# Optimization experiments

Hardware: AMD Instinct MI355X
Metric: run time of the kernel (lower is better)

The kernel has to match this reference:

```python
import jax, jax.numpy as jnp
import numpy as np

N_NODES = 100000
N_EDGES = 1600000
F_IN = 128
F_OUT = 128


def _spmm(edge_row, edge_col, edge_weight, X):
    # sparse [N,N] @ dense [N,F]: gather source rows, weight, scatter-add to dest rows
    msgs = edge_weight[:, None] * X[edge_col]  # [E, F]
    return jax.ops.segment_sum(msgs, edge_row, num_segments=N_NODES)


def setup_inputs() -> dict:
    key = jax.random.key(0)
    ks = jax.random.split(key, 7)
    scale = 1.0 / np.sqrt(F_IN)
    return {
        "x": jax.random.normal(ks[0], (N_NODES, F_IN), dtype=jnp.float32),
        "edge_row": jax.random.randint(ks[1], (N_EDGES,), 0, N_NODES, dtype=jnp.int32),
        "edge_col": jax.random.randint(ks[2], (N_EDGES,), 0, N_NODES, dtype=jnp.int32),
        "edge_weight": jax.random.uniform(ks[3], (N_EDGES,), dtype=jnp.float32),
        "w1": jax.random.normal(ks[4], (F_IN, F_IN), dtype=jnp.float32) * scale,
        "w2": jax.random.normal(ks[5], (F_IN, F_OUT), dtype=jnp.float32) * scale,
        "w3": jax.random.normal(ks[6], (F_OUT, F_OUT), dtype=jnp.float32) * scale,
    }


def reference(x, edge_row, edge_col, edge_weight, w1, w2, w3):
    # dropout p=0.0 (eval) -> identity
    h = jax.nn.relu(_spmm(edge_row, edge_col, edge_weight, x @ w1))
    h = jax.nn.relu(_spmm(edge_row, edge_col, edge_weight, h @ w2))
    h = jax.nn.relu(_spmm(edge_row, edge_col, edge_weight, h @ w3))
    return h
```

## Files before the change

### kernel.cpp

```cpp
#include <hip/hip_runtime.h>

#define N_NODES 100000
#define N_EDGES 1600000
#define F 128

#define SCAN_B 1024
#define SCAN_NB ((N_NODES + SCAN_B - 1) / SCAN_B)

typedef short bf16x8 __attribute__((ext_vector_type(8)));
typedef float f32x4  __attribute__((ext_vector_type(4)));

union ABFrag {
    bf16x8 v;
    unsigned short u[8];
    uint4  q;
};

__device__ __forceinline__ unsigned short f2bf(float f) {
    unsigned int u = __float_as_uint(f);
    u += 0x7fffu + ((u >> 16) & 1u);
    return (unsigned short)(u >> 16);
}
__device__ __forceinline__ float bflo(unsigned int u) {
    return __uint_as_float(u << 16);
}
__device__ __forceinline__ float bfhi(unsigned int u) {
    return __uint_as_float(u & 0xFFFF0000u);
}


__global__ void edge_histogram(const int* __restrict__ erow, int* __restrict__ counts) {
    const int e = blockIdx.x * blockDim.x + threadIdx.x;
    atomicAdd(&counts[erow[e]], 1);
}

__global__ void scan_block_sums(const int* __restrict__ counts, int* __restrict__ bsums) {
    __shared__ int s[SCAN_B];
    const int t = threadIdx.x;
    const int idx = blockIdx.x * SCAN_B + t;
    int v = (idx < N_NODES) ? counts[idx] : 0;
    s[t] = v;
    __syncthreads();
    for (int off = SCAN_B / 2; off > 0; off >>= 1) {
        if (t < off) s[t] += s[t + off];
        __syncthreads();
    }
    if (t == 0) bsums[blockIdx.x] = s[0];
}

__global__ void scan_bsums(const int* __restrict__ bsums, int* __restrict__ boffs) {
    __shared__ int s[128];
    const int t = threadIdx.x;
    int v = (t < SCAN_NB) ? bsums[t] : 0;
    s[t] = v;
    __syncthreads();
    for (int off = 1; off < 128; off <<= 1) {
        int u = (t >= off) ? s[t - off] : 0;
        __syncthreads();
        s[t] += u;
        __syncthreads();
    }
    if (t < SCAN_NB) boffs[t] = s[t] - v;
}

__global__ void scan_final(const int* __restrict__ counts, const int* __restrict__ boffs,
                           int* __restrict__ row_ptr) {
    __shared__ int s[SCAN_B];
    const int t = threadIdx.x;
    const int idx = blockIdx.x * SCAN_B + t;
    int v = (idx < N_NODES) ? counts[idx] : 0;
    s[t] = v;
    __syncthreads();
    for (int off = 1; off < SCAN_B; off <<= 1) {
        int u = (t >= off) ? s[t - off] : 0;
        __syncthreads();
        s[t] += u;
        __syncthreads();
    }
    if (idx < N_NODES) row_ptr[idx] = boffs[blockIdx.x] + s[t] - v;
    if (idx == 0) row_ptr[N_NODES] = N_EDGES;
}

__global__ void csr_fill(const int* __restrict__ erow, const int* __restrict__ ecol,
                         const float* __restrict__ ewgt,
                         const int* __restrict__ row_ptr, int* __restrict__ cursor,
                         unsigned int* __restrict__ pairs) {
    const int e = blockIdx.x * blockDim.x + threadIdx.x;
    const int dst = erow[e];
    const int pos = atomicAdd(&cursor[dst], 1);
    pairs[row_ptr[dst] + pos] = ((unsigned int)ecol[e] << 15) | (unsigned int)f2bf(ewgt[e]);
}

__global__ void transpose_w_bf16(const float* __restrict__ W, unsigned short* __restrict__ Wt) {
    const int i = blockIdx.x * 256 + threadIdx.x;
    const int n = i >> 7;
    const int k = i & 127;
    Wt[i] = f2bf(W[k * F + n]);
}

__global__ __launch_bounds__(256) void gemm_mfma(
    const float* __restrict__ Xf,
    const unsigned short* __restrict__ Xb,
    const unsigned short* __restrict__ Wt,
    unsigned short* __restrict__ Y,
    int use_f32_in)
{
    __shared__ unsigned short Wl[4 * 8 * 64 * 8];

    const int tid  = threadIdx.x;
    const int wave = tid >> 6;
    const int lane = tid & 63;

    for (int s = tid; s < 2048; s += 256) {
        const int ln  = s & 63;
        const int ntk = s >> 6;
        const int nt  = ntk & 7;
        const int kt  = ntk >> 3;
        const int n   = nt * 16 + (ln & 15);
        const int k   = kt * 32 + (ln >> 4) * 8;
        *(uint4*)(&Wl[s * 8]) = *(const uint4*)(Wt + n * F + k);
    }
    __syncthreads();

    const int m     = blockIdx.x * 64 + wave * 16 + (lane & 15);
    const bool mval = (m < N_NODES);
    const int kq    = (lane >> 4) * 8;

    f32x4 acc[8] = {};

#pragma unroll
    for (int kt = 0; kt < 4; ++kt) {
        ABFrag a;
        if (mval) {
            if (use_f32_in) {
                const float* p = Xf + (size_t)m * F + kt * 32 + kq;
                const float4 u0 = *(const float4*)p;
                const float4 u1 = *(const float4*)(p + 4);
                a.u[0] = f2bf(u0.x); a.u[1] = f2bf(u0.y);
                a.u[2] = f2bf(u0.z); a.u[3] = f2bf(u0.w);
                a.u[4] = f2bf(u1.x); a.u[5] = f2bf(u1.y);
                a.u[6] = f2bf(u1.z); a.u[7] = f2bf(u1.w);
            } else {
                a.q = *(const uint4*)(Xb + (size_t)m * F + kt * 32 + kq);
#pragma unroll
                for (int j = 0; j < 8; ++j)
                    if (a.u[j] & 0x8000u) a.u[j] = 0;
            }
        } else {
            a.q = make_uint4(0, 0, 0, 0);
        }
#pragma unroll
        for (int nt = 0; nt < 8; ++nt) {
            ABFrag b;
            b.q = *(const uint4*)(&Wl[((kt * 8 + nt) * 64 + lane) * 8]);
            acc[nt] = __builtin_amdgcn_mfma_f32_16x16x32_bf16(a.v, b.v, acc[nt], 0, 0, 0);
        }
    }

    const int rbase = blockIdx.x * 64 + wave * 16 + (lane >> 4) * 4;
    const int cbase = lane & 15;
#pragma unroll
    for (int r = 0; r < 4; ++r) {
        const int row = rbase + r;
        if (row < N_NODES) {
#pragma unroll
            for (int nt = 0; nt < 8; ++nt) {
                Y[(size_t)row * F + nt * 16 + cbase] = f2bf(acc[nt][r]);
            }
        }
    }
}

__global__ __launch_bounds__(256) void spmm_csr_bf16(
    const unsigned short* __restrict__ Xb,
    const int* __restrict__ row_ptr,
    const unsigned int* __restrict__ pairs,
    unsigned short* __restrict__ Ob,
    float* __restrict__ Of,
    int final_mode) {
    const int tid = threadIdx.x;
    const int l16 = tid & 15;
    const int q   = tid >> 4;
    const int row = blockIdx.x * 16 + q;

    const int beg = row_ptr[row];
    const int end = row_ptr[row + 1];

    float a[8] = {};
    int i = beg;
    for (; i + 1 < end; i += 2) {
        const unsigned int p0 = pairs[i], p1 = pairs[i + 1];
        const uint4 v0 = *(const uint4*)(Xb + (size_t)(p0 >> 15) * F + l16 * 8);
        const uint4 v1 = *(const uint4*)(Xb + (size_t)(p1 >> 15) * F + l16 * 8);
        const float w0 = bflo(p0 & 0x7FFFu);
        const float w1 = bflo(p1 & 0x7FFFu);
        a[0] += w0 * bflo(v0.x); a[1] += w0 * bfhi(v0.x);
        a[2] += w0 * bflo(v0.y); a[3] += w0 * bfhi(v0.y);
        a[4] += w0 * bflo(v0.z); a[5] += w0 * bfhi(v0.z);
        a[6] += w0 * bflo(v0.w); a[7] += w0 * bfhi(v0.w);
        a[0] += w1 * bflo(v1.x); a[1] += w1 * bfhi(v1.x);
        a[2] += w1 * bflo(v1.y); a[3] += w1 * bfhi(v1.y);
        a[4] += w1 * bflo(v1.z); a[5] += w1 * bfhi(v1.z);
        a[6] += w1 * bflo(v1.w); a[7] += w1 * bfhi(v1.w);
    }
    if (i < end) {
        const unsigned int p0 = pairs[i];
        const uint4 v0 = *(const uint4*)(Xb + (size_t)(p0 >> 15) * F + l16 * 8);
        const float w0 = bflo(p0 & 0x7FFFu);
        a[0] += w0 * bflo(v0.x); a[1] += w0 * bfhi(v0.x);
        a[2] += w0 * bflo(v0.y); a[3] += w0 * bfhi(v0.y);
        a[4] += w0 * bflo(v0.z); a[5] += w0 * bfhi(v0.z);
        a[6] += w0 * bflo(v0.w); a[7] += w0 * bfhi(v0.w);
    }

    if (final_mode) {
        float4 o0 = {fmaxf(a[0], 0.f), fmaxf(a[1], 0.f), fmaxf(a[2], 0.f), fmaxf(a[3], 0.f)};
        float4 o1 = {fmaxf(a[4], 0.f), fmaxf(a[5], 0.f), fmaxf(a[6], 0.f), fmaxf(a[7], 0.f)};
        float* p = Of + (size_t)row * F + l16 * 8;
        *(float4*)p = o0;
        *(float4*)(p + 4) = o1;
    } else {
        uint4 o;
        o.x = (unsigned int)f2bf(a[0]) | ((unsigned int)f2bf(a[1]) << 16);
        o.y = (unsigned int)f2bf(a[2]) | ((unsigned int)f2bf(a[3]) << 16);
        o.z = (unsigned int)f2bf(a[4]) | ((unsigned int)f2bf(a[5]) << 16);
        o.w = (unsigned int)f2bf(a[6]) | ((unsigned int)f2bf(a[7]) << 16);
        *(uint4*)(Ob + (size_t)row * F + l16 * 8) = o;
    }
}


extern "C" void kernel_launch(void* const* d_in, const int* in_sizes, int n_in,
                              void* d_out, int out_size, void* d_ws, size_t ws_size,
                              hipStream_t stream) {
    const float* x    = (const float*)d_in[0];
    const int*   erow = (const int*)d_in[1];
    const int*   ecol = (const int*)d_in[2];
    const float* ew   = (const float*)d_in[3];
    const float* w1   = (const float*)d_in[4];
    const float* w2   = (const float*)d_in[5];
    const float* w3   = (const float*)d_in[6];
    float* out = (float*)d_out;

    char* ws = (char*)d_ws;
    size_t off = 0;
    auto alloc = [&](size_t bytes) -> char* {
        char* p = ws + off;
        off += (bytes + 255) & ~(size_t)255;
        return p;
    };
    unsigned short* bufA = (unsigned short*)alloc((size_t)N_NODES * F * 2);
    unsigned short* bufB = (unsigned short*)alloc((size_t)N_NODES * F * 2);
    unsigned int* pairs  = (unsigned int*)alloc((size_t)N_EDGES * 4);
    int* counts  = (int*)alloc((size_t)N_NODES * sizeof(int));
    int* row_ptr = (int*)alloc(((size_t)N_NODES + 1) * sizeof(int));
    int* bsums   = (int*)alloc((size_t)SCAN_NB * sizeof(int));
    int* boffs   = (int*)alloc((size_t)SCAN_NB * sizeof(int));
    unsigned short* wt1 = (unsigned short*)alloc((size_t)F * F * 2);
    unsigned short* wt2 = (unsigned short*)alloc((size_t)F * F * 2);
    unsigned short* wt3 = (unsigned short*)alloc((size_t)F * F * 2);

    hipMemsetAsync(counts, 0, (size_t)N_NODES * sizeof(int), stream);
    edge_histogram<<<N_EDGES / 256, 256, 0, stream>>>(erow, counts);
    scan_block_sums<<<SCAN_NB, SCAN_B, 0, stream>>>(counts, bsums);
    scan_bsums<<<1, 128, 0, stream>>>(bsums, boffs);
    scan_final<<<SCAN_NB, SCAN_B, 0, stream>>>(counts, boffs, row_ptr);
    hipMemsetAsync(counts, 0, (size_t)N_NODES * sizeof(int), stream);
    csr_fill<<<N_EDGES / 256, 256, 0, stream>>>(erow, ecol, ew, row_ptr, counts, pairs);

    transpose_w_bf16<<<64, 256, 0, stream>>>(w1, wt1);
    transpose_w_bf16<<<64, 256, 0, stream>>>(w2, wt2);
    transpose_w_bf16<<<64, 256, 0, stream>>>(w3, wt3);

    const int ggrid = (N_NODES + 63) / 64;
    const int sgrid = N_NODES / 16;

    gemm_mfma<<<ggrid, 256, 0, stream>>>(x, nullptr, wt1, bufA, 1);
    spmm_csr_bf16<<<sgrid, 256, 0, stream>>>(bufA, row_ptr, pairs, bufB, nullptr, 0);
    gemm_mfma<<<ggrid, 256, 0, stream>>>(nullptr, bufB, wt2, bufA, 0);
    spmm_csr_bf16<<<sgrid, 256, 0, stream>>>(bufA, row_ptr, pairs, bufB, nullptr, 0);
    gemm_mfma<<<ggrid, 256, 0, stream>>>(nullptr, bufB, wt3, bufA, 0);
    spmm_csr_bf16<<<sgrid, 256, 0, stream>>>(bufA, row_ptr, pairs, nullptr, out, 1);
}
```

Before: 506.3 us.

## Partition CSR build atomics by XCD, widen GEMM tiles, unroll SpMM by four

```diff
diff --git a/kernel.cpp b/kernel.cpp
--- a/kernel.cpp
+++ b/kernel.cpp
@@ -3,17 +3,19 @@
 #define N_NODES 100000
 #define N_EDGES 1600000
 #define F 128
+#define XCD_RANGE 12500
 
 #define SCAN_B 1024
 #define SCAN_NB ((N_NODES + SCAN_B - 1) / SCAN_B)
 
 typedef short bf16x8 __attribute__((ext_vector_type(8)));
 typedef float f32x4  __attribute__((ext_vector_type(4)));
+typedef unsigned int u32x4 __attribute__((ext_vector_type(4)));
 
 union ABFrag {
     bf16x8 v;
     unsigned short u[8];
-    uint4  q;
+    u32x4  q;
 };
 
 __device__ __forceinline__ unsigned short f2bf(float f) {
@@ -29,9 +31,15 @@
 }
 
 
-__global__ void edge_histogram(const int* __restrict__ erow, int* __restrict__ counts) {
-    const int e = blockIdx.x * blockDim.x + threadIdx.x;
-    atomicAdd(&counts[erow[e]], 1);
+__global__ __launch_bounds__(256) void edge_histogram_xcd(
+    const int* __restrict__ erow, int* __restrict__ counts) {
+    const int xcd = blockIdx.x & 7;
+    const int e   = (blockIdx.x >> 3) * 256 + threadIdx.x;
+    const int dst = erow[e];
+    const int lo  = xcd * XCD_RANGE;
+    if (dst >= lo && dst < lo + XCD_RANGE) {
+        atomicAdd(&counts[dst], 1);
+    }
 }
 
 __global__ void scan_block_sums(const int* __restrict__ counts, int* __restrict__ bsums) {
@@ -81,21 +89,32 @@
     if (idx == 0) row_ptr[N_NODES] = N_EDGES;
 }
 
-__global__ void csr_fill(const int* __restrict__ erow, const int* __restrict__ ecol,
-                         const float* __restrict__ ewgt,
-                         const int* __restrict__ row_ptr, int* __restrict__ cursor,
-                         unsigned int* __restrict__ pairs) {
-    const int e = blockIdx.x * blockDim.x + threadIdx.x;
+__global__ __launch_bounds__(256) void csr_fill_xcd(
+    const int* __restrict__ erow, const int* __restrict__ ecol,
+    const float* __restrict__ ewgt,
+    const int* __restrict__ row_ptr, int* __restrict__ cursor,
+    unsigned int* __restrict__ pairs) {
+    const int xcd = blockIdx.x & 7;
+    const int e   = (blockIdx.x >> 3) * 256 + threadIdx.x;
     const int dst = erow[e];
-    const int pos = atomicAdd(&cursor[dst], 1);
-    pairs[row_ptr[dst] + pos] = ((unsigned int)ecol[e] << 15) | (unsigned int)f2bf(ewgt[e]);
-}
-
-__global__ void transpose_w_bf16(const float* __restrict__ W, unsigned short* __restrict__ Wt) {
+    const int lo  = xcd * XCD_RANGE;
+    if (dst >= lo && dst < lo + XCD_RANGE) {
+        const int col = ecol[e];
+        const float w = ewgt[e];
+        const int pos = atomicAdd(&cursor[dst], 1);
+        pairs[row_ptr[dst] + pos] = ((unsigned int)col << 15) | (unsigned int)f2bf(w);
+    }
+}
+
+__global__ void transpose_w3(const float* __restrict__ w1, const float* __restrict__ w2,
+                             const float* __restrict__ w3, unsigned short* __restrict__ wt) {
     const int i = blockIdx.x * 256 + threadIdx.x;
-    const int n = i >> 7;
-    const int k = i & 127;
-    Wt[i] = f2bf(W[k * F + n]);
+    const int which = i >> 14;
+    const int j = i & 16383;
+    const float* W = (which == 0) ? w1 : (which == 1) ? w2 : w3;
+    const int n = j >> 7;
+    const int k = j & 127;
+    wt[i] = f2bf(W[k * F + n]);
 }
 
 __global__ __launch_bounds__(256) void gemm_mfma(
@@ -118,54 +137,77 @@
         const int kt  = ntk >> 3;
         const int n   = nt * 16 + (ln & 15);
         const int k   = kt * 32 + (ln >> 4) * 8;
-        *(uint4*)(&Wl[s * 8]) = *(const uint4*)(Wt + n * F + k);
+        *(u32x4*)(&Wl[s * 8]) = *(const u32x4*)(Wt + n * F + k);
     }
     __syncthreads();
 
-    const int m     = blockIdx.x * 64 + wave * 16 + (lane & 15);
-    const bool mval = (m < N_NODES);
-    const int kq    = (lane >> 4) * 8;
-
-    f32x4 acc[8] = {};
+    const int kq = (lane >> 4) * 8;
+    const int m0 = blockIdx.x * 128 + wave * 16 + (lane & 15);
+    const int m1 = m0 + 64;
+    const bool v0 = (m0 < N_NODES);
+    const bool v1 = (m1 < N_NODES);
+
+    f32x4 acc[2][8] = {};
 
 #pragma unroll
     for (int kt = 0; kt < 4; ++kt) {
-        ABFrag a;
-        if (mval) {
-            if (use_f32_in) {
-                const float* p = Xf + (size_t)m * F + kt * 32 + kq;
+        ABFrag a0, a1;
+        a0.q = 0;
+        a1.q = 0;
+        if (use_f32_in) {
+            if (v0) {
+                const float* p = Xf + (size_t)m0 * F + kt * 32 + kq;
                 const float4 u0 = *(const float4*)p;
                 const float4 u1 = *(const float4*)(p + 4);
-                a.u[0] = f2bf(u0.x); a.u[1] = f2bf(u0.y);
-                a.u[2] = f2bf(u0.z); a.u[3] = f2bf(u0.w);
-                a.u[4] = f2bf(u1.x); a.u[5] = f2bf(u1.y);
-                a.u[6] = f2bf(u1.z); a.u[7] = f2bf(u1.w);
-            } else {
-                a.q = *(const uint4*)(Xb + (size_t)m * F + kt * 32 + kq);
+                a0.u[0] = f2bf(u0.x); a0.u[1] = f2bf(u0.y);
+                a0.u[2] = f2bf(u0.z); a0.u[3] = f2bf(u0.w);
+                a0.u[4] = f2bf(u1.x); a0.u[5] = f2bf(u1.y);
+                a0.u[6] = f2bf(u1.z); a0.u[7] = f2bf(u1.w);
+            }
+            if (v1) {
+                const float* p = Xf + (size_t)m1 * F + kt * 32 + kq;
+                const float4 u0 = *(const float4*)p;
+                const float4 u1 = *(const float4*)(p + 4);
+                a1.u[0] = f2bf(u0.x); a1.u[1] = f2bf(u0.y);
+                a1.u[2] = f2bf(u0.z); a1.u[3] = f2bf(u0.w);
+                a1.u[4] = f2bf(u1.x); a1.u[5] = f2bf(u1.y);
+                a1.u[6] = f2bf(u1.z); a1.u[7] = f2bf(u1.w);
+            }
+        } else {
+            if (v0) {
+                a0.q = *(const u32x4*)(Xb + (size_t)m0 * F + kt * 32 + kq);
 #pragma unroll
                 for (int j = 0; j < 8; ++j)
-                    if (a.u[j] & 0x8000u) a.u[j] = 0;
-            }
-        } else {
-            a.q = make_uint4(0, 0, 0, 0);
+                    if (a0.u[j] & 0x8000u) a0.u[j] = 0;
+            }
+            if (v1) {
+                a1.q = *(const u32x4*)(Xb + (size_t)m1 * F + kt * 32 + kq);
+#pragma unroll
+                for (int j = 0; j < 8; ++j)
+                    if (a1.u[j] & 0x8000u) a1.u[j] = 0;
+            }
         }
 #pragma unroll
         for (int nt = 0; nt < 8; ++nt) {
             ABFrag b;
-            b.q = *(const uint4*)(&Wl[((kt * 8 + nt) * 64 + lane) * 8]);
-            acc[nt] = __builtin_amdgcn_mfma_f32_16x16x32_bf16(a.v, b.v, acc[nt], 0, 0, 0);
+            b.q = *(const u32x4*)(&Wl[((kt * 8 + nt) * 64 + lane) * 8]);
+            acc[0][nt] = __builtin_amdgcn_mfma_f32_16x16x32_bf16(a0.v, b.v, acc[0][nt], 0, 0, 0);
+            acc[1][nt] = __builtin_amdgcn_mfma_f32_16x16x32_bf16(a1.v, b.v, acc[1][nt], 0, 0, 0);
         }
     }
 
-    const int rbase = blockIdx.x * 64 + wave * 16 + (lane >> 4) * 4;
     const int cbase = lane & 15;
 #pragma unroll
-    for (int r = 0; r < 4; ++r) {
-        const int row = rbase + r;
-        if (row < N_NODES) {
-#pragma unroll
-            for (int nt = 0; nt < 8; ++nt) {
-                Y[(size_t)row * F + nt * 16 + cbase] = f2bf(acc[nt][r]);
+    for (int t = 0; t < 2; ++t) {
+        const int rbase = blockIdx.x * 128 + t * 64 + wave * 16 + (lane >> 4) * 4;
+#pragma unroll
+        for (int r = 0; r < 4; ++r) {
+            const int row = rbase + r;
+            if (row < N_NODES) {
+#pragma unroll
+                for (int nt = 0; nt < 8; ++nt) {
+                    Y[(size_t)row * F + nt * 16 + cbase] = f2bf(acc[t][nt][r]);
+                }
             }
         }
     }
@@ -188,12 +230,19 @@
 
     float a[8] = {};
     int i = beg;
-    for (; i + 1 < end; i += 2) {
-        const unsigned int p0 = pairs[i], p1 = pairs[i + 1];
-        const uint4 v0 = *(const uint4*)(Xb + (size_t)(p0 >> 15) * F + l16 * 8);
-        const uint4 v1 = *(const uint4*)(Xb + (size_t)(p1 >> 15) * F + l16 * 8);
+    for (; i + 3 < end; i += 4) {
+        const unsigned int p0 = __builtin_nontemporal_load(&pairs[i]);
+        const unsigned int p1 = __builtin_nontemporal_load(&pairs[i + 1]);
+        const unsigned int p2 = __builtin_nontemporal_load(&pairs[i + 2]);
+        const unsigned int p3 = __builtin_nontemporal_load(&pairs[i + 3]);
+        const u32x4 v0 = *(const u32x4*)(Xb + (size_t)(p0 >> 15) * F + l16 * 8);
+        const u32x4 v1 = *(const u32x4*)(Xb + (size_t)(p1 >> 15) * F + l16 * 8);
+        const u32x4 v2 = *(const u32x4*)(Xb + (size_t)(p2 >> 15) * F + l16 * 8);
+        const u32x4 v3 = *(const u32x4*)(Xb + (size_t)(p3 >> 15) * F + l16 * 8);
         const float w0 = bflo(p0 & 0x7FFFu);
         const float w1 = bflo(p1 & 0x7FFFu);
+        const float w2 = bflo(p2 & 0x7FFFu);
+        const float w3 = bflo(p3 & 0x7FFFu);
         a[0] += w0 * bflo(v0.x); a[1] += w0 * bfhi(v0.x);
         a[2] += w0 * bflo(v0.y); a[3] += w0 * bfhi(v0.y);
         a[4] += w0 * bflo(v0.z); a[5] += w0 * bfhi(v0.z);
@@ -202,10 +251,18 @@
         a[2] += w1 * bflo(v1.y); a[3] += w1 * bfhi(v1.y);
         a[4] += w1 * bflo(v1.z); a[5] += w1 * bfhi(v1.z);
         a[6] += w1 * bflo(v1.w); a[7] += w1 * bfhi(v1.w);
-    }
-    if (i < end) {
-        const unsigned int p0 = pairs[i];
-        const uint4 v0 = *(const uint4*)(Xb + (size_t)(p0 >> 15) * F + l16 * 8);
+        a[0] += w2 * bflo(v2.x); a[1] += w2 * bfhi(v2.x);
+        a[2] += w2 * bflo(v2.y); a[3] += w2 * bfhi(v2.y);
+        a[4] += w2 * bflo(v2.z); a[5] += w2 * bfhi(v2.z);
+        a[6] += w2 * bflo(v2.w); a[7] += w2 * bfhi(v2.w);
+        a[0] += w3 * bflo(v3.x); a[1] += w3 * bfhi(v3.x);
+        a[2] += w3 * bflo(v3.y); a[3] += w3 * bfhi(v3.y);
+        a[4] += w3 * bflo(v3.z); a[5] += w3 * bfhi(v3.z);
+        a[6] += w3 * bflo(v3.w); a[7] += w3 * bfhi(v3.w);
+    }
+    for (; i < end; ++i) {
+        const unsigned int p0 = __builtin_nontemporal_load(&pairs[i]);
+        const u32x4 v0 = *(const u32x4*)(Xb + (size_t)(p0 >> 15) * F + l16 * 8);
         const float w0 = bflo(p0 & 0x7FFFu);
         a[0] += w0 * bflo(v0.x); a[1] += w0 * bfhi(v0.x);
         a[2] += w0 * bflo(v0.y); a[3] += w0 * bfhi(v0.y);
@@ -214,18 +271,18 @@
     }
 
     if (final_mode) {
-        float4 o0 = {fmaxf(a[0], 0.f), fmaxf(a[1], 0.f), fmaxf(a[2], 0.f), fmaxf(a[3], 0.f)};
-        float4 o1 = {fmaxf(a[4], 0.f), fmaxf(a[5], 0.f), fmaxf(a[6], 0.f), fmaxf(a[7], 0.f)};
+        f32x4 o0 = {fmaxf(a[0], 0.f), fmaxf(a[1], 0.f), fmaxf(a[2], 0.f), fmaxf(a[3], 0.f)};
+        f32x4 o1 = {fmaxf(a[4], 0.f), fmaxf(a[5], 0.f), fmaxf(a[6], 0.f), fmaxf(a[7], 0.f)};
         float* p = Of + (size_t)row * F + l16 * 8;
-        *(float4*)p = o0;
-        *(float4*)(p + 4) = o1;
+        __builtin_nontemporal_store(o0, (f32x4*)p);
+        __builtin_nontemporal_store(o1, (f32x4*)(p + 4));
     } else {
-        uint4 o;
+        u32x4 o;
         o.x = (unsigned int)f2bf(a[0]) | ((unsigned int)f2bf(a[1]) << 16);
         o.y = (unsigned int)f2bf(a[2]) | ((unsigned int)f2bf(a[3]) << 16);
         o.z = (unsigned int)f2bf(a[4]) | ((unsigned int)f2bf(a[5]) << 16);
         o.w = (unsigned int)f2bf(a[6]) | ((unsigned int)f2bf(a[7]) << 16);
-        *(uint4*)(Ob + (size_t)row * F + l16 * 8) = o;
+        __builtin_nontemporal_store(o, (u32x4*)(Ob + (size_t)row * F + l16 * 8));
     }
 }
 
@@ -252,27 +309,26 @@
     unsigned short* bufA = (unsigned short*)alloc((size_t)N_NODES * F * 2);
     unsigned short* bufB = (unsigned short*)alloc((size_t)N_NODES * F * 2);
     unsigned int* pairs  = (unsigned int*)alloc((size_t)N_EDGES * 4);
-    int* counts  = (int*)alloc((size_t)N_NODES * sizeof(int));
+    int* counts  = (int*)alloc((size_t)N_NODES * sizeof(int) * 2);
+    int* cursor  = counts + N_NODES;
     int* row_ptr = (int*)alloc(((size_t)N_NODES + 1) * sizeof(int));
     int* bsums   = (int*)alloc((size_t)SCAN_NB * sizeof(int));
     int* boffs   = (int*)alloc((size_t)SCAN_NB * sizeof(int));
-    unsigned short* wt1 = (unsigned short*)alloc((size_t)F * F * 2);
-    unsigned short* wt2 = (unsigned short*)alloc((size_t)F * F * 2);
-    unsigned short* wt3 = (unsigned short*)alloc((size_t)F * F * 2);
-
-    hipMemsetAsync(counts, 0, (size_t)N_NODES * sizeof(int), stream);
-    edge_histogram<<<N_EDGES / 256, 256, 0, stream>>>(erow, counts);
+    unsigned short* wt = (unsigned short*)alloc((size_t)3 * F * F * 2);
+    unsigned short* wt1 = wt;
+    unsigned short* wt2 = wt + F * F;
+    unsigned short* wt3 = wt + 2 * F * F;
+
+    hipMemsetAsync(counts, 0, (size_t)N_NODES * sizeof(int) * 2, stream);
+    edge_histogram_xcd<<<8 * (N_EDGES / 256), 256, 0, stream>>>(erow, counts);
     scan_block_sums<<<SCAN_NB, SCAN_B, 0, stream>>>(counts, bsums);
     scan_bsums<<<1, 128, 0, stream>>>(bsums, boffs);
     scan_final<<<SCAN_NB, SCAN_B, 0, stream>>>(counts, boffs, row_ptr);
-    hipMemsetAsync(counts, 0, (size_t)N_NODES * sizeof(int), stream);
-    csr_fill<<<N_EDGES / 256, 256, 0, stream>>>(erow, ecol, ew, row_ptr, counts, pairs);
-
-    transpose_w_bf16<<<64, 256, 0, stream>>>(w1, wt1);
-    transpose_w_bf16<<<64, 256, 0, stream>>>(w2, wt2);
-    transpose_w_bf16<<<64, 256, 0, stream>>>(w3, wt3);
-
-    const int ggrid = (N_NODES + 63) / 64;
+    csr_fill_xcd<<<8 * (N_EDGES / 256), 256, 0, stream>>>(erow, ecol, ew, row_ptr, cursor, pairs);
+
+    transpose_w3<<<192, 256, 0, stream>>>(w1, w2, w3, wt);
+
+    const int ggrid = (N_NODES + 127) / 128;
     const int sgrid = N_NODES / 16;
 
     gemm_mfma<<<ggrid, 256, 0, stream>>>(x, nullptr, wt1, bufA, 1);
```

After: 509.1 us. No clear change (+0.6%).
